# Performance work log

Hardware: AMD Instinct MI355X
Metric: run time of the kernel (lower is better)

## Reference

```python
import jax, jax.numpy as jnp
import numpy as np

S = 8          # num_slots
DSLOT = 128    # slot_dim
D_IN = 768     # input feature dim
ITERS = 3      # slot_att_iter
RES = 21       # 336 // 16
NGRID = RES * RES   # 441 grid positions
NTOK = 441          # tokens kept per frame (no drop here)
NFRAME = 2
F_ = 2 * NFRAME + 1  # 5 frames per clip
CLIPS = 8
B = CLIPS * F_       # 40
SIGMA = 5.0
SCALE = DSLOT ** -0.5
EPS = 1e-8


def layernorm(x, g, b):
    m = x.mean(-1, keepdims=True)
    v = ((x - m) ** 2).mean(-1, keepdims=True)
    return (x - m) * jax.lax.rsqrt(v + 1e-5) * g + b


def setup_inputs() -> dict:
    key = jax.random.key(0)
    ks = iter(jax.random.split(key, 64))
    def nrm(shape, s=0.02):
        return jax.random.normal(next(ks), shape, jnp.float32) * s
    xs = jnp.linspace(-1.0, 1.0, RES)
    ys = jnp.linspace(-1.0, 1.0, RES)
    gx, gy = jnp.meshgrid(xs, ys)  # indexing='xy' as in torch
    abs_grid = jnp.stack([gx.ravel(), gy.ravel()], axis=-1)  # [NGRID, 2]
    return {
        "inputs": jax.random.normal(next(ks), (B, NTOK, D_IN), jnp.float32),
        "token_indices": jnp.sort(jax.random.randint(next(ks), (B, NTOK), 0, NGRID), axis=-1),
        "abs_grid": abs_grid,
        "slots_init": nrm((1, S, DSLOT), 0.1),
        "S_p_init": nrm((1, S, 1, 2), 0.02),
        "S_s_init": jax.random.uniform(next(ks), (1, S, 1, 2), jnp.float32, 0.3, 0.7),
        "WQ": nrm((DSLOT, DSLOT)), "ln_g": jnp.ones((DSLOT,)), "ln_b": jnp.zeros((DSLOT,)),
        "gru_w_ih": nrm((DSLOT, 3 * DSLOT)), "gru_w_hh": nrm((DSLOT, 3 * DSLOT)),
        "gru_b_ih": jnp.zeros((3 * DSLOT,)), "gru_b_hh": jnp.zeros((3 * DSLOT,)),
        "mlp_ln_g": jnp.ones((DSLOT,)), "mlp_ln_b": jnp.zeros((DSLOT,)),
        "mlp_w1": nrm((DSLOT, 4 * DSLOT)), "mlp_b1": jnp.zeros((4 * DSLOT,)),
        "mlp_w2": nrm((4 * DSLOT, DSLOT)), "mlp_b2": jnp.zeros((DSLOT,)),
        "WK": nrm((DSLOT, DSLOT)), "WV": nrm((DSLOT, DSLOT)),
        "Wg": nrm((2, DSLOT)), "bg": jnp.zeros((DSLOT,)),
        "Wf1": nrm((DSLOT, DSLOT)), "bf1": jnp.zeros((DSLOT,)),
        "Wf2": nrm((DSLOT, DSLOT)), "bf2": jnp.zeros((DSLOT,)),
        "im_ln1_g": jnp.ones((D_IN,)), "im_ln1_b": jnp.zeros((D_IN,)),
        "im_w1": nrm((D_IN, D_IN)), "im_b1": jnp.zeros((D_IN,)),
        "im_w2": nrm((D_IN, DSLOT)), "im_b2": jnp.zeros((DSLOT,)),
        "im_ln2_g": jnp.ones((DSLOT,)), "im_ln2_b": jnp.zeros((DSLOT,)),
        "fin_w": nrm((DSLOT, DSLOT)), "fin_b": jnp.zeros((DSLOT,)),
    }


def _forward(inputs, token_indices, abs_grid, slots_init, S_p_init, S_s_init,
             WQ, ln_g, ln_b, gru_w_ih, gru_w_hh, gru_b_ih, gru_b_hh,
             mlp_ln_g, mlp_ln_b, mlp_w1, mlp_b1, mlp_w2, mlp_b2,
             WK, WV, Wg, bg, Wf1, bf1, Wf2, bf2,
             im_ln1_g, im_ln1_b, im_w1, im_b1, im_w2, im_b2, im_ln2_g, im_ln2_b,
             fin_w, fin_b):
    Bb = inputs.shape[0]
    # initial_mlp: LN -> Linear -> ReLU -> Linear -> LN
    x = layernorm(inputs, im_ln1_g, im_ln1_b)
    x = jax.nn.relu(x @ im_w1 + im_b1)
    x = x @ im_w2 + im_b2
    x = layernorm(x, im_ln2_g, im_ln2_b)          # [B, N, Dslot]
    # K/V projections of inputs are slot-independent; compute once.
    Kx = x @ WK                                    # [B, N, Dslot]
    Vx = x @ WV
    ag = abs_grid[token_indices]                   # [B, N, 2] per-batch gather
    slots = jnp.broadcast_to(slots_init, (Bb, S, DSLOT))
    S_p = jnp.broadcast_to(S_p_init, (Bb, S, 1, 2))
    S_s = jnp.broadcast_to(S_s_init, (Bb, S, 1, 2))

    def f_net(z):  # f = Linear -> ReLU -> Linear
        return jax.nn.relu(z @ Wf1 + bf1) @ Wf2 + bf2

    attn = None
    for t in range(ITERS + 1):
        slots_prev = slots
        sn = layernorm(slots, ln_g, ln_b)
        rel = (ag[:, None] - S_p) / (S_s * SIGMA)  # [B, S, N, 2]
        gr = rel @ Wg + bg                          # [B, S, N, Dslot]
        k = f_net(Kx[:, None] + gr)
        v = f_net(Vx[:, None] + gr)
        q = sn @ WQ                                 # [B, S, Dslot]
        dots = jnp.einsum('bsd,bsjd->bsj', q, k) * SCALE
        attn = jax.nn.softmax(dots, axis=1) + EPS   # softmax over slots
        attn = attn / attn.sum(-1, keepdims=True)   # renormalize over tokens
        updates = jnp.einsum('bsjd,bsj->bsd', v, attn)
        S_p = jnp.einsum('bjd,bsj->bsd', ag, attn)[:, :, None, :]
        S_s = jnp.sqrt(jnp.einsum('bsjd,bsj->bsd', (ag[:, None] - S_p) ** 2, attn))[:, :, None, :]
        if t != ITERS:
            # torch GRUCell
            xg = updates.reshape(-1, DSLOT)
            hg = slots_prev.reshape(-1, DSLOT)
            gi = xg @ gru_w_ih + gru_b_ih
            gh = hg @ gru_w_hh + gru_b_hh
            i_r, i_z, i_n = jnp.split(gi, 3, axis=-1)
            h_r, h_z, h_n = jnp.split(gh, 3, axis=-1)
            r = jax.nn.sigmoid(i_r + h_r)
            z = jax.nn.sigmoid(i_z + h_z)
            n = jnp.tanh(i_n + r * h_n)
            slots = ((1.0 - z) * n + z * hg).reshape(Bb, S, DSLOT)
            # residual pre-LN MLP (dropout is identity in eval)
            y = layernorm(slots, mlp_ln_g, mlp_ln_b)
            y = jax.nn.relu(y @ mlp_w1 + mlp_b1) @ mlp_w2 + mlp_b2
            slots = slots + y
    slots = slots @ fin_w + fin_b
    attn_out = attn.reshape(-1, F_, S, NTOK)[:, NFRAME]  # center frame
    return slots, attn_out


def reference(inputs, token_indices, abs_grid, slots_init, S_p_init, S_s_init,
              WQ, ln_g, ln_b, gru_w_ih, gru_w_hh, gru_b_ih, gru_b_hh,
              mlp_ln_g, mlp_ln_b, mlp_w1, mlp_b1, mlp_w2, mlp_b2,
              WK, WV, Wg, bg, Wf1, bf1, Wf2, bf2,
              im_ln1_g, im_ln1_b, im_w1, im_b1, im_w2, im_b2, im_ln2_g, im_ln2_b,
              fin_w, fin_b):
    return _forward(inputs, token_indices, abs_grid, slots_init, S_p_init, S_s_init,
                    WQ, ln_g, ln_b, gru_w_ih, gru_w_hh, gru_b_ih, gru_b_hh,
                    mlp_ln_g, mlp_ln_b, mlp_w1, mlp_b1, mlp_w2, mlp_b2,
                    WK, WV, Wg, bg, Wf1, bf1, Wf2, bf2,
                    im_ln1_g, im_ln1_b, im_w1, im_b1, im_w2, im_b2, im_ln2_g, im_ln2_b,
                    fin_w, fin_b)
```

## Files before the change

kernel.cpp:

```cpp
#include <hip/hip_runtime.h>
#include <cstdio>

#define NB 40
#define NS 8
#define NT 441
#define DIN 768
#define DD 128
#define NTOT (NB*NT)
#define FSCALE 0.08838834764831843f

typedef short s8v __attribute__((ext_vector_type(8)));
typedef float f4v __attribute__((ext_vector_type(4)));

__device__ inline ushort f2bf(float f){
  unsigned u = __float_as_uint(f);
  unsigned r = (u + 0x7fffu + ((u >> 16) & 1u)) >> 16;
  return (ushort)r;
}
__device__ inline float bf2f(ushort h){ return __uint_as_float(((unsigned)h) << 16); }
__device__ inline float dot4a(float4 a, float4 b, float acc){
  return fmaf(a.w, b.w, fmaf(a.z, b.z, fmaf(a.y, b.y, fmaf(a.x, b.x, acc))));
}

struct PP {
  const float *inputs; const int *tok_idx; const float *abs_grid;
  const float *slots_init, *Sp_init, *Ss_init;
  const float *WQ, *ln_g, *ln_b;
  const float *gru_w_ih, *gru_w_hh, *gru_b_ih, *gru_b_hh;
  const float *mlp_ln_g, *mlp_ln_b, *mlp_w1, *mlp_b1, *mlp_w2, *mlp_b2;
  const float *WK, *WV, *Wg, *bg, *Wf1, *bf1, *Wf2, *bf2;
  const float *im_ln1_g, *im_ln1_b, *im_w1, *im_b1, *im_w2, *im_b2, *im_ln2_g, *im_ln2_b;
  const float *fin_w, *fin_b;
  float *A_K, *A_V, *Wg1, *c1, *Wf2T;
  float *slots_g, *qw_g, *qb_g, *spss_g, *hpart_g, *a_g;
  float4 *WQp, *f2P, *f2TP, *finP, *gihP, *ghhP, *w1P, *w2P;
  ushort *xnh, *xnl, *hh, *hl, *W1Th, *W1Tl, *W2Th, *W2Tl;
  ushort *WKfTh, *WKfTl, *WVfTh, *WVfTl;
  float *out;
};

__global__ __launch_bounds__(128) void prep_weights(PP p){
  int r = blockIdx.x, d = threadIdx.x;
  float accK = 0.f, accV = 0.f;
  for (int kk = 0; kk < DD; kk++){
    float w = p.Wf1[kk*DD + d];
    accK = fmaf(p.WK[r*DD+kk], w, accK);
    accV = fmaf(p.WV[r*DD+kk], w, accV);
  }
  ushort hk = f2bf(accK), hv = f2bf(accV);
  p.WKfTh[d*DD + r] = hk; p.WKfTl[d*DD + r] = f2bf(accK - bf2f(hk));
  p.WVfTh[d*DD + r] = hv; p.WVfTl[d*DD + r] = f2bf(accV - bf2f(hv));
  if (r < 2){
    float a = 0.f;
    for (int kk = 0; kk < DD; kk++) a = fmaf(p.Wg[r*DD+kk], p.Wf1[kk*DD+d], a);
    p.Wg1[r*DD+d] = a;
  }
  if (r == 2){
    float a = 0.f;
    for (int kk = 0; kk < DD; kk++) a = fmaf(p.bg[kk], p.Wf1[kk*DD+d], a);
    p.c1[d] = a + p.bf1[d];
  }
  p.Wf2T[d*DD + r] = p.Wf2[r*DD + d];
}

__global__ __launch_bounds__(256) void prep_pack(PP p){
  long i = (long)blockIdx.x*256 + threadIdx.x;
  const float* src; float4* dst; int N; long base;
  if      (i < 4096) { src = p.WQ;        dst = p.WQp;  N = 128; base = 0; }
  else if (i < 8192) { src = p.Wf2;       dst = p.f2P;  N = 128; base = 4096; }
  else if (i < 12288){ src = p.Wf2T;      dst = p.f2TP; N = 128; base = 8192; }
  else if (i < 16384){ src = p.fin_w;     dst = p.finP; N = 128; base = 12288; }
  else if (i < 28672){ src = p.gru_w_ih;  dst = p.gihP; N = 384; base = 16384; }
  else if (i < 40960){ src = p.gru_w_hh;  dst = p.ghhP; N = 384; base = 28672; }
  else if (i < 57344){ src = p.mlp_w1;    dst = p.w1P;  N = 512; base = 40960; }
  else               { src = p.mlp_w2;    dst = p.w2P;  N = 128; base = 57344; }
  long j = i - base;
  long k4 = j / N, o = j % N;
  float4 v;
  v.x = src[(k4*4+0)*N+o]; v.y = src[(k4*4+1)*N+o];
  v.z = src[(k4*4+2)*N+o]; v.w = src[(k4*4+3)*N+o];
  dst[j] = v;
}

__global__ __launch_bounds__(256) void transpose_both(PP p){
  __shared__ float tile[64][65];
  int t = blockIdx.x;
  const float* W; ushort *WTh, *WTl; int N, k0, n0;
  if (t < 144){ W = p.im_w1; WTh = p.W1Th; WTl = p.W1Tl; N = 768; k0 = (t/12)*64; n0 = (t%12)*64; }
  else { t -= 144; W = p.im_w2; WTh = p.W2Th; WTl = p.W2Tl; N = 128; k0 = (t/2)*64; n0 = (t&1)*64; }
  int tid = threadIdx.x;
  #pragma unroll
  for (int i = 0; i < 4; i++){
    int k = i*16 + (tid >> 4);
    int n4 = (tid & 15) * 4;
    float4 v = *(const float4*)(W + (long)(k0+k)*N + n0 + n4);
    tile[k][n4+0] = v.x; tile[k][n4+1] = v.y; tile[k][n4+2] = v.z; tile[k][n4+3] = v.w;
  }
  __syncthreads();
  #pragma unroll
  for (int i = 0; i < 4; i++){
    int n = i*16 + (tid >> 4);
    int k4 = (tid & 15) * 4;
    ushort4 h4, l4;
    float v0 = tile[k4+0][n], v1 = tile[k4+1][n], v2 = tile[k4+2][n], v3 = tile[k4+3][n];
    h4.x = f2bf(v0); l4.x = f2bf(v0 - bf2f(h4.x));
    h4.y = f2bf(v1); l4.y = f2bf(v1 - bf2f(h4.y));
    h4.z = f2bf(v2); l4.z = f2bf(v2 - bf2f(h4.z));
    h4.w = f2bf(v3); l4.w = f2bf(v3 - bf2f(h4.w));
    *(ushort4*)(WTh + (long)(n0+n)*DIN + k0 + k4) = h4;
    *(ushort4*)(WTl + (long)(n0+n)*DIN + k0 + k4) = l4;
  }
}

__device__ void phase0g(const PP& p, int bs, int tid, float* scr, const float* sl,
                        float Sp0, float Sp1, float Ss0, float Ss1){
  float* sn   = scr;
  float* qv   = scr + 128;
  float* part = scr + 256;
  float* red  = scr + 512;
  int o = tid & 127, h = tid >> 7;
  float v = (tid < 128) ? sl[tid] : 0.f;
  float s1 = v, s2 = v*v;
  #pragma unroll
  for (int m = 1; m < 64; m <<= 1){ s1 += __shfl_xor(s1,m); s2 += __shfl_xor(s2,m); }
  if (tid < 128 && (tid & 63) == 0){ red[(tid>>6)*2] = s1; red[(tid>>6)*2+1] = s2; }
  __syncthreads();
  float mean = (red[0]+red[2])*(1.f/128.f);
  float var  = (red[1]+red[3])*(1.f/128.f) - mean*mean;
  float rstd = rsqrtf(var + 1e-5f);
  if (tid < 128) sn[tid] = (v-mean)*rstd*p.ln_g[tid] + p.ln_b[tid];
  __syncthreads();
  float acc = 0.f;
  for (int k4 = 0; k4 < 16; k4++){
    float4 sv = *(const float4*)&sn[h*64 + k4*4];
    float4 wv = p.WQp[(h*16 + k4)*128 + o];
    acc = dot4a(sv, wv, acc);
  }
  part[h*128+o] = acc;
  __syncthreads();
  if (tid < 128) qv[tid] = part[tid] + part[128+tid];
  __syncthreads();
  float acc2 = 0.f;
  for (int k4 = 0; k4 < 16; k4++){
    float4 qv4 = *(const float4*)&qv[h*64 + k4*4];
    float4 wv  = p.f2TP[(h*16 + k4)*128 + o];
    acc2 = dot4a(qv4, wv, acc2);
  }
  part[h*128+o] = acc2;
  __syncthreads();
  if (tid < 128) p.qw_g[(long)bs*128+tid] = part[tid] + part[128+tid];
  float pb = (tid < 128) ? qv[tid]*p.bf2[tid] : 0.f;
  #pragma unroll
  for (int m = 1; m < 64; m <<= 1) pb += __shfl_xor(pb,m);
  if ((tid & 63) == 0) red[4 + (tid>>6)] = pb;
  __syncthreads();
  if (tid == 0){
    p.qb_g[bs] = FSCALE*(red[4]+red[5]+red[6]+red[7]);
    p.spss_g[bs*4+0] = Sp0; p.spss_g[bs*4+1] = Sp1;
    p.spss_g[bs*4+2] = 1.f/(Ss0*5.0f); p.spss_g[bs*4+3] = 1.f/(Ss1*5.0f);
  }
}

__global__ __launch_bounds__(256) void ln1_init(PP p){
  __shared__ __align__(16) float sl[128];
  __shared__ __align__(16) float scr[520];
  if (blockIdx.x < 4410){
    int tok = blockIdx.x*4 + (threadIdx.x >> 6);
    int l = threadIdx.x & 63;
    const float* src = p.inputs + (long)tok*DIN;
    float4 v[3];
    float s = 0.f, s2 = 0.f;
    #pragma unroll
    for (int pp = 0; pp < 3; pp++){
      v[pp] = *(const float4*)(src + pp*256 + l*4);
      s  += v[pp].x + v[pp].y + v[pp].z + v[pp].w;
      s2 += v[pp].x*v[pp].x + v[pp].y*v[pp].y + v[pp].z*v[pp].z + v[pp].w*v[pp].w;
    }
    #pragma unroll
    for (int m = 1; m < 64; m <<= 1){ s += __shfl_xor(s, m); s2 += __shfl_xor(s2, m); }
    float mean = s*(1.f/DIN), var = s2*(1.f/DIN) - mean*mean;
    float rstd = rsqrtf(var + 1e-5f);
    #pragma unroll
    for (int pp = 0; pp < 3; pp++){
      int idx = pp*256 + l*4;
      float4 g = *(const float4*)(p.im_ln1_g + idx);
      float4 b = *(const float4*)(p.im_ln1_b + idx);
      float y0 = (v[pp].x-mean)*rstd*g.x + b.x;
      float y1 = (v[pp].y-mean)*rstd*g.y + b.y;
      float y2 = (v[pp].z-mean)*rstd*g.z + b.z;
      float y3 = (v[pp].w-mean)*rstd*g.w + b.w;
      ushort4 h4, l4;
      h4.x = f2bf(y0); l4.x = f2bf(y0 - bf2f(h4.x));
      h4.y = f2bf(y1); l4.y = f2bf(y1 - bf2f(h4.y));
      h4.z = f2bf(y2); l4.z = f2bf(y2 - bf2f(h4.z));
      h4.w = f2bf(y3); l4.w = f2bf(y3 - bf2f(h4.w));
      *(ushort4*)(p.xnh + (long)tok*DIN + idx) = h4;
      *(ushort4*)(p.xnl + (long)tok*DIN + idx) = l4;
    }
  } else {
    int bs = blockIdx.x - 4410, ss = bs & 7, tid = threadIdx.x;
    if (tid < 128){
      float v = p.slots_init[ss*128+tid];
      sl[tid] = v;
      p.slots_g[(long)bs*128+tid] = v;
    }
    __syncthreads();
    phase0g(p, bs, tid, scr, sl,
            p.Sp_init[ss*2], p.Sp_init[ss*2+1], p.Ss_init[ss*2], p.Ss_init[ss*2+1]);
  }
}

__global__ __launch_bounds__(256, 2) void gemm1_128(PP p){
  __shared__ __align__(16) ushort LDSm[32768];
  int id = blockIdx.x;
  int xcd = id & 7, idx = id >> 3;
  int m_t = xcd + 8*(idx/6), n_t = idx % 6;
  if (m_t >= 138) return;
  int m0 = m_t*128, n0 = n_t*128;
  int tid = threadIdx.x;
  int w = tid >> 6, lane = tid & 63;
  int wm = w >> 1, wn = w & 1;
  int lch = lane ^ ((lane >> 3) & 7);
  int r_in = lch >> 2, kgs = lch & 3;
  const ushort* S = (w == 0) ? p.xnh : (w == 1) ? p.xnl : (w == 2) ? p.W1Th : p.W1Tl;
  int base0 = (w < 2) ? m0 : n0;
  bool isA = (w < 2);
  int kg = lane >> 4, rA = lane & 15;
  int cc = rA*4 + kg;
  int cs = cc ^ ((cc >> 3) & 7);
  const char* LB = (const char*)LDSm;

  f4v acc[4][4];
  #pragma unroll
  for (int mf = 0; mf < 4; mf++)
    #pragma unroll
    for (int nf = 0; nf < 4; nf++) acc[mf][nf] = (f4v)(0.f);

  #pragma unroll
  for (int t = 0; t < 8; t++){
    int grow = base0 + t*16 + r_in;
    if (isA) grow = min(grow, NTOT-1);
    const ushort* gptr = S + (long)grow*DIN + 0 + kgs*8;
    ushort* lptr = &LDSm[w*4096 + t*512];
    __builtin_amdgcn_global_load_lds(
        (const __attribute__((address_space(1))) void*)gptr,
        (__attribute__((address_space(3))) void*)lptr, 16, 0, 0);
  }
  __syncthreads();

  int cur = 0;
  for (int kb = 0; kb < DIN; kb += 32){
    if (kb + 32 < DIN){
      int nb = cur ^ 1;
      #pragma unroll
      for (int t = 0; t < 8; t++){
        int grow = base0 + t*16 + r_in;
        if (isA) grow = min(grow, NTOT-1);
        const ushort* gptr = S + (long)grow*DIN + (kb + 32) + kgs*8;
        ushort* lptr = &LDSm[nb*16384 + w*4096 + t*512];
        __builtin_amdgcn_global_load_lds(
            (const __attribute__((address_space(1))) void*)gptr,
            (__attribute__((address_space(3))) void*)lptr, 16, 0, 0);
      }
    }
    const char* B = LB + cur*32768;
    s8v a0[4], a1[4], b0[4], b1[4];
    #pragma unroll
    for (int mf = 0; mf < 4; mf++){
      int win = wm*4 + mf;
      a0[mf] = *(const s8v*)(B +         win*1024 + cs*16);
      a1[mf] = *(const s8v*)(B +  8192 + win*1024 + cs*16);
    }
    #pragma unroll
    for (int nf = 0; nf < 4; nf++){
      int win = wn*4 + nf;
      b0[nf] = *(const s8v*)(B + 16384 + win*1024 + cs*16);
      b1[nf] = *(const s8v*)(B + 24576 + win*1024 + cs*16);
    }
    #pragma unroll
    for (int mf = 0; mf < 4; mf++)
      #pragma unroll
      for (int nf = 0; nf < 4; nf++){
        acc[mf][nf] = __builtin_amdgcn_mfma_f32_16x16x32_bf16(a0[mf], b0[nf], acc[mf][nf], 0, 0, 0);
        acc[mf][nf] = __builtin_amdgcn_mfma_f32_16x16x32_bf16(a0[mf], b1[nf], acc[mf][nf], 0, 0, 0);
        acc[mf][nf] = __builtin_amdgcn_mfma_f32_16x16x32_bf16(a1[mf], b0[nf], acc[mf][nf], 0, 0, 0);
      }
    __syncthreads();
    cur ^= 1;
  }

  int rbase = (lane >> 4) * 4, cn = lane & 15;
  #pragma unroll
  for (int mf = 0; mf < 4; mf++)
    #pragma unroll
    for (int nf = 0; nf < 4; nf++){
      int n = n0 + wn*64 + nf*16 + cn;
      float bs = p.im_b1[n];
      #pragma unroll
      for (int r = 0; r < 4; r++){
        int m = m0 + wm*64 + mf*16 + rbase + r;
        if (m < NTOT){
          float v = fmaxf(acc[mf][nf][r] + bs, 0.f);
          ushort h = f2bf(v);
          p.hh[(long)m*DIN + n] = h;
          p.hl[(long)m*DIN + n] = f2bf(v - bf2f(h));
        }
      }
    }
}

__global__ __launch_bounds__(256) void gemm2_fused(PP p){
  __shared__ __align__(16) char smem[43008];
  ushort* As = (ushort*)smem;
  ushort* Bs = (ushort*)(smem + 5120);
  float*  Dl = (float*)smem;
  ushort* xsh = (ushort*)(smem + 25600);
  ushort* xsl = (ushort*)(smem + 25600 + 8704);
  int m0 = blockIdx.x * 32;
  int tid = threadIdx.x, w = tid >> 6, lane = tid & 63;
  f4v acc[2][2];
  #pragma unroll
  for (int mf = 0; mf < 2; mf++)
    #pragma unroll
    for (int nf = 0; nf < 2; nf++) acc[mf][nf] = (f4v)(0.f);

  for (int kb = 0; kb < DIN; kb += 32){
    __syncthreads();
    {
      int c = tid;
      int s = c >> 7, rem = c & 127, r = rem >> 2, kg = rem & 3;
      int gr = min(m0 + r, NTOT-1);
      const float4 va = *(const float4*)((s ? p.hl : p.hh) + (long)gr*DIN + kb + kg*8);
      *(float4*)(As + s*1280 + r*40 + kg*8) = va;
    }
    #pragma unroll
    for (int i = 0; i < 4; i++){
      int c = tid + i*256;
      int s = c >> 9, r = (c >> 2) & 127, kg = c & 3;
      const float4 vb = *(const float4*)((s ? p.W2Tl : p.W2Th) + (long)r*DIN + kb + kg*8);
      *(float4*)(Bs + s*5120 + r*40 + kg*8) = vb;
    }
    __syncthreads();
    int kg = lane >> 4, rA = lane & 15;
    s8v a0[2], a1[2], b0[2], b1[2];
    #pragma unroll
    for (int mf = 0; mf < 2; mf++){
      a0[mf] = *(const s8v*)(As +        (mf*16 + rA)*40 + kg*8);
      a1[mf] = *(const s8v*)(As + 1280 + (mf*16 + rA)*40 + kg*8);
    }
    #pragma unroll
    for (int nf = 0; nf < 2; nf++){
      int rb = w*32 + nf*16 + rA;
      b0[nf] = *(const s8v*)(Bs +        rb*40 + kg*8);
      b1[nf] = *(const s8v*)(Bs + 5120 + rb*40 + kg*8);
    }
    #pragma unroll
    for (int mf = 0; mf < 2; mf++)
      #pragma unroll
      for (int nf = 0; nf < 2; nf++){
        acc[mf][nf] = __builtin_amdgcn_mfma_f32_16x16x32_bf16(a0[mf], b0[nf], acc[mf][nf], 0, 0, 0);
        acc[mf][nf] = __builtin_amdgcn_mfma_f32_16x16x32_bf16(a0[mf], b1[nf], acc[mf][nf], 0, 0, 0);
        acc[mf][nf] = __builtin_amdgcn_mfma_f32_16x16x32_bf16(a1[mf], b0[nf], acc[mf][nf], 0, 0, 0);
      }
  }

  int rbase = (lane >> 4) * 4, cn = lane & 15;
  __syncthreads();
  #pragma unroll
  for (int mf = 0; mf < 2; mf++)
    #pragma unroll
    for (int nf = 0; nf < 2; nf++){
      int n = w*32 + nf*16 + cn;
      float bs = p.im_b2[n];
      #pragma unroll
      for (int r = 0; r < 4; r++)
        Dl[(mf*16 + rbase + r)*132 + n] = acc[mf][nf][r] + bs;
    }
  __syncthreads();
  for (int rr = 0; rr < 8; rr++){
    int row = w*8 + rr;
    float e0 = Dl[row*132 + lane], e1 = Dl[row*132 + 64 + lane];
    float s = e0 + e1, s2 = e0*e0 + e1*e1;
    #pragma unroll
    for (int m2 = 1; m2 < 64; m2 <<= 1){ s += __shfl_xor(s, m2); s2 += __shfl_xor(s2, m2); }
    float mean = s*(1.f/DD), var = s2*(1.f/DD) - mean*mean;
    float rstd = rsqrtf(var + 1e-5f);
    float x0 = (e0-mean)*rstd*p.im_ln2_g[lane]    + p.im_ln2_b[lane];
    float x1 = (e1-mean)*rstd*p.im_ln2_g[64+lane] + p.im_ln2_b[64+lane];
    ushort h0 = f2bf(x0), h1 = f2bf(x1);
    xsh[row*136 + lane]      = h0;  xsl[row*136 + lane]      = f2bf(x0 - bf2f(h0));
    xsh[row*136 + 64 + lane] = h1;  xsl[row*136 + 64 + lane] = f2bf(x1 - bf2f(h1));
  }
  __syncthreads();
  int kg = lane >> 4, rA = lane & 15;
  int kv = w >> 1, rowblk = w & 1;
  const ushort* WTh = kv ? p.WVfTh : p.WKfTh;
  const ushort* WTl = kv ? p.WVfTl : p.WKfTl;
  float* OUT = kv ? p.A_V : p.A_K;
  f4v aO[8];
  #pragma unroll
  for (int nf = 0; nf < 8; nf++) aO[nf] = (f4v)(0.f);
  #pragma unroll
  for (int kb2 = 0; kb2 < 4; kb2++){
    s8v ah = *(const s8v*)&xsh[(rowblk*16+rA)*136 + kb2*32 + kg*8];
    s8v al = *(const s8v*)&xsl[(rowblk*16+rA)*136 + kb2*32 + kg*8];
    #pragma unroll
    for (int nf = 0; nf < 8; nf++){
      int n = nf*16 + rA;
      s8v bh = *(const s8v*)(WTh + n*DD + kb2*32 + kg*8);
      s8v bl = *(const s8v*)(WTl + n*DD + kb2*32 + kg*8);
      aO[nf] = __builtin_amdgcn_mfma_f32_16x16x32_bf16(ah, bh, aO[nf], 0, 0, 0);
      aO[nf] = __builtin_amdgcn_mfma_f32_16x16x32_bf16(ah, bl, aO[nf], 0, 0, 0);
      aO[nf] = __builtin_amdgcn_mfma_f32_16x16x32_bf16(al, bh, aO[nf], 0, 0, 0);
    }
  }
  #pragma unroll
  for (int nf = 0; nf < 8; nf++){
    int n = nf*16 + cn;
    float c = p.c1[n];
    #pragma unroll
    for (int r = 0; r < 4; r++){
      int m = m0 + rowblk*16 + rbase + r;
      if (m < NTOT) OUT[(long)m*DD + n] = aO[nf][r] + c;
    }
  }
}

template<int LAST>
__global__ __launch_bounds__(256) void kA(PP p){
  int b = blockIdx.x / 7, tile = blockIdx.x % 7;
  int tid = threadIdx.x, wid = tid >> 6, lane = tid & 63;
  __shared__ float qws[8][132];
  __shared__ float qbs[8];
  __shared__ float spssL[32];
  __shared__ float agt[64][2];
  __shared__ float a_tile[8][64];
  __shared__ float hpartL[4][8][128];
  for (int f = tid; f < 8*128; f += 256){
    int s = f >> 7, d = f & 127;
    qws[s][(d&31)*4 + (d>>5)] = p.qw_g[((long)b*8+s)*128 + d];
  }
  if (tid < 8)  qbs[tid] = p.qb_g[b*8+tid];
  if (tid < 32) spssL[tid] = p.spss_g[b*32+tid];
  if (tid < 64){
    int j = tile*64 + tid;
    float g0 = 0.f, g1 = 0.f;
    if (j < NT){ int idx = p.tok_idx[b*NT+j]; g0 = p.abs_grid[idx*2]; g1 = p.abs_grid[idx*2+1]; }
    agt[tid][0] = g0; agt[tid][1] = g1;
  }
  __syncthreads();

  {
    int tl = lane >> 2, dg = lane & 3;
    int jtok = wid*16 + tl, j = tile*64 + jtok;
    bool valid = j < NT;
    int jc = valid ? j : 0;
    float aa[32], w0[32], w1[32];
    const float* src = p.A_K + ((long)(b*NT+jc))*DD + dg*32;
    #pragma unroll
    for (int i4 = 0; i4 < 8; i4++){
      float4 t = *(const float4*)(src + i4*4);
      aa[i4*4+0]=t.x; aa[i4*4+1]=t.y; aa[i4*4+2]=t.z; aa[i4*4+3]=t.w;
    }
    #pragma unroll
    for (int i4 = 0; i4 < 8; i4++){
      float4 t0 = *(const float4*)(p.Wg1 + dg*32 + i4*4);
      float4 t1 = *(const float4*)(p.Wg1 + DD + dg*32 + i4*4);
      w0[i4*4+0]=t0.x; w0[i4*4+1]=t0.y; w0[i4*4+2]=t0.z; w0[i4*4+3]=t0.w;
      w1[i4*4+0]=t1.x; w1[i4*4+1]=t1.y; w1[i4*4+2]=t1.z; w1[i4*4+3]=t1.w;
    }
    float ag0 = agt[jtok][0], ag1 = agt[jtok][1];
    float dv[8];
    #pragma unroll
    for (int s = 0; s < 8; s++){
      float rel0 = (ag0 - spssL[s*4+0])*spssL[s*4+2];
      float rel1 = (ag1 - spssL[s*4+1])*spssL[s*4+3];
      float acc = 0.f;
      #pragma unroll
      for (int i = 0; i < 32; i++){
        float hk = fmaxf(fmaf(rel0, w0[i], fmaf(rel1, w1[i], aa[i])), 0.f);
        acc = fmaf(hk, qws[s][i*4+dg], acc);
      }
      acc += __shfl_xor(acc, 1); acc += __shfl_xor(acc, 2);
      dv[s] = acc*FSCALE + qbs[s];
    }
    if (dg == 0){
      float m = -1e30f;
      #pragma unroll
      for (int s = 0; s < 8; s++) m = fmaxf(m, dv[s]);
      float tot = 0.f;
      #pragma unroll
      for (int s = 0; s < 8; s++){ dv[s] = expf(dv[s]-m); tot += dv[s]; }
      float inv = 1.f/tot;
      #pragma unroll
      for (int s = 0; s < 8; s++)
        a_tile[s][jtok] = valid ? (dv[s]*inv + 1e-8f) : 0.f;
    }
  }
  __syncthreads();

  #pragma unroll
  for (int si = 0; si < 2; si++){
    int s = wid*2 + si;
    float a = a_tile[s][lane];
    float g0 = agt[lane][0], g1 = agt[lane][1];
    float v0 = a, v1 = a*g0, v2 = a*g1, v3 = a*g0*g0, v4 = a*g1*g1;
    #pragma unroll
    for (int m = 1; m < 64; m <<= 1){
      v0 += __shfl_xor(v0,m); v1 += __shfl_xor(v1,m); v2 += __shfl_xor(v2,m);
      v3 += __shfl_xor(v3,m); v4 += __shfl_xor(v4,m);
    }
    if (lane == 0){
      float* st = p.hpart_g + ((long)(b*7+tile)*8 + s)*136 + 128;
      st[0]=v0; st[1]=v1; st[2]=v2; st[3]=v3; st[4]=v4;
    }
  }

  if (LAST){
    if ((b % 5) == 2){
      int clip = b/5;
      for (int f = tid; f < 8*64; f += 256){
        int s = f >> 6, jt = f & 63;
        int j = tile*64 + jt;
        if (j < NT) p.a_g[((long)clip*8 + s)*NT + j] = a_tile[s][jt];
      }
    }
    return;
  }

  {
    float sp0[8], sp1[8], si0[8], si1[8];
    #pragma unroll
    for (int s = 0; s < 8; s++){
      sp0[s]=spssL[s*4+0]; sp1[s]=spssL[s*4+1]; si0[s]=spssL[s*4+2]; si1[s]=spssL[s*4+3];
    }
    int d0 = lane, d1 = lane + 64;
    float wg0a = p.Wg1[d0], wg1a = p.Wg1[DD+d0];
    float wg0b = p.Wg1[d1], wg1b = p.Wg1[DD+d1];
    float acc0[8], acc1[8];
    #pragma unroll
    for (int s = 0; s < 8; s++){ acc0[s]=0.f; acc1[s]=0.f; }
    for (int jj = wid; jj < 64; jj += 4){
      int j = tile*64 + jj;
      if (j >= NT) continue;
      float av0 = p.A_V[((long)(b*NT+j))*DD + d0];
      float av1 = p.A_V[((long)(b*NT+j))*DD + d1];
      float g0 = agt[jj][0], g1 = agt[jj][1];
      #pragma unroll
      for (int s = 0; s < 8; s++){
        float rel0 = (g0 - sp0[s])*si0[s];
        float rel1 = (g1 - sp1[s])*si1[s];
        float a = a_tile[s][jj];
        float hv0 = fmaxf(fmaf(rel0, wg0a, fmaf(rel1, wg1a, av0)), 0.f);
        float hv1 = fmaxf(fmaf(rel0, wg0b, fmaf(rel1, wg1b, av1)), 0.f);
        acc0[s] = fmaf(a, hv0, acc0[s]);
        acc1[s] = fmaf(a, hv1, acc1[s]);
      }
    }
    #pragma unroll
    for (int s = 0; s < 8; s++){ hpartL[wid][s][d0] = acc0[s]; hpartL[wid][s][d1] = acc1[s]; }
    __syncthreads();
    for (int f = tid; f < 1024; f += 256){
      int s = f >> 7, d = f & 127;
      p.hpart_g[((long)(b*7+tile)*8 + s)*136 + d] =
        hpartL[0][s][d] + hpartL[1][s][d] + hpartL[2][s][d] + hpartL[3][s][d];
    }
  }
}

template<int LAST>
__global__ __launch_bounds__(256) void kB(PP p){
  __shared__ __align__(16) float red[8];
  __shared__ __align__(16) float sl[128];
  __shared__ __align__(16) float hb[128];
  __shared__ __align__(16) float scr[2304];
  int bs = blockIdx.x, b = bs >> 3, ss = bs & 7, tid = threadIdx.x;
  if (tid < 5){
    float v = 0.f;
    #pragma unroll
    for (int t7 = 0; t7 < 7; t7++) v += p.hpart_g[((long)(b*7+t7)*8 + ss)*136 + 128 + tid];
    red[tid] = v;
  }
  __syncthreads();
  float SA = red[0], inv = 1.f/SA;
  float Sp0 = red[1]*inv, Sp1 = red[2]*inv;
  float Ss0 = sqrtf(fmaxf(red[3]*inv - Sp0*Sp0, 0.f));
  float Ss1 = sqrtf(fmaxf(red[4]*inv - Sp1*Sp1, 0.f));

  if (LAST){
    if ((b % 5) == 2){
      int clip = b/5;
      long base = (long)NB*NS*DD + ((long)clip*8 + ss)*NT;
      const float* arow = p.a_g + ((long)clip*8 + ss)*NT;
      for (int j = tid; j < NT; j += 256) p.out[base+j] = arow[j]*inv;
    }
    if (tid < 128) sl[tid] = p.slots_g[(long)bs*128+tid];
    __syncthreads();
    int o = tid & 127, h = tid >> 7;
    float acc = 0.f;
    for (int k4 = 0; k4 < 16; k4++){
      float4 sv = *(const float4*)&sl[h*64 + k4*4];
      float4 wv = p.finP[(h*16 + k4)*128 + o];
      acc = dot4a(sv, wv, acc);
    }
    scr[h*128+o] = acc;
    __syncthreads();
    if (tid < 128) p.out[(long)bs*128+tid] = p.fin_b[tid] + scr[tid] + scr[128+tid];
    return;
  }

  if (tid < 128){
    float v = 0.f;
    #pragma unroll
    for (int t7 = 0; t7 < 7; t7++) v += p.hpart_g[((long)(b*7+t7)*8 + ss)*136 + tid];
    hb[tid] = v * inv;
    sl[tid] = p.slots_g[(long)bs*128+tid];
  }
  __syncthreads();
  float* part = scr;
  float* upd  = scr + 256;
  float* gil  = scr + 384;
  float* ghl  = scr + 768;
  float* hnl  = scr + 1152;
  float* yv   = scr + 1280;
  float* h1   = scr + 1408;
  int o = tid & 127, h = tid >> 7;
  float acc2 = 0.f;
  for (int k4 = 0; k4 < 16; k4++){
    float4 hv = *(const float4*)&hb[h*64 + k4*4];
    float4 wv = p.f2P[(h*16 + k4)*128 + o];
    acc2 = dot4a(hv, wv, acc2);
  }
  part[h*128+o] = acc2;
  __syncthreads();
  if (tid < 128) upd[tid] = part[tid] + part[128+tid] + p.bf2[tid];
  __syncthreads();
  int oA = tid, oB = tid + 256;
  float giA = p.gru_b_ih[oA], ghA = p.gru_b_hh[oA];
  float giB = 0.f, ghB = 0.f;
  if (tid < 128){ giB = p.gru_b_ih[oB]; ghB = p.gru_b_hh[oB]; }
  for (int k4 = 0; k4 < 32; k4++){
    float4 u4 = *(const float4*)&upd[k4*4];
    float4 s4 = *(const float4*)&sl[k4*4];
    float4 wiA = p.gihP[k4*384 + oA];
    float4 whA = p.ghhP[k4*384 + oA];
    giA = dot4a(u4, wiA, giA);
    ghA = dot4a(s4, whA, ghA);
    if (tid < 128){
      float4 wiB = p.gihP[k4*384 + oB];
      float4 whB = p.ghhP[k4*384 + oB];
      giB = dot4a(u4, wiB, giB);
      ghB = dot4a(s4, whB, ghB);
    }
  }
  gil[oA] = giA; ghl[oA] = ghA;
  if (tid < 128){ gil[oB] = giB; ghl[oB] = ghB; }
  __syncthreads();
  float hnv = 0.f;
  if (tid < 128){
    float r = 1.f/(1.f+expf(-(gil[tid]+ghl[tid])));
    float z = 1.f/(1.f+expf(-(gil[128+tid]+ghl[128+tid])));
    float n = tanhf(gil[256+tid] + r*ghl[256+tid]);
    hnv = (1.f-z)*n + z*sl[tid];
  }
  float t1 = hnv, t2 = hnv*hnv;
  #pragma unroll
  for (int m = 1; m < 64; m <<= 1){ t1 += __shfl_xor(t1,m); t2 += __shfl_xor(t2,m); }
  if (tid < 128 && (tid & 63) == 0){ red[(tid>>6)*2] = t1; red[(tid>>6)*2+1] = t2; }
  __syncthreads();
  float mean = (red[0]+red[2])*(1.f/128.f);
  float var  = (red[1]+red[3])*(1.f/128.f) - mean*mean;
  float rstd = rsqrtf(var + 1e-5f);
  if (tid < 128){
    hnl[tid] = hnv;
    yv[tid] = (hnv-mean)*rstd*p.mlp_ln_g[tid] + p.mlp_ln_b[tid];
  }
  __syncthreads();
  float m1A = p.mlp_b1[tid], m1B = p.mlp_b1[tid+256];
  for (int k4 = 0; k4 < 32; k4++){
    float4 y4 = *(const float4*)&yv[k4*4];
    float4 wA = p.w1P[k4*512 + tid];
    float4 wB = p.w1P[k4*512 + tid + 256];
    m1A = dot4a(y4, wA, m1A);
    m1B = dot4a(y4, wB, m1B);
  }
  h1[tid] = fmaxf(m1A, 0.f); h1[tid+256] = fmaxf(m1B, 0.f);
  __syncthreads();
  float a2 = 0.f;
  for (int k4 = 0; k4 < 64; k4++){
    float4 h4 = *(const float4*)&h1[h*256 + k4*4];
    float4 wv = p.w2P[(h*64 + k4)*128 + o];
    a2 = dot4a(h4, wv, a2);
  }
  part[h*128+o] = a2;
  __syncthreads();
  if (tid < 128){
    float sln = hnl[tid] + p.mlp_b2[tid] + part[tid] + part[128+tid];
    sl[tid] = sln;
    p.slots_g[(long)bs*128+tid] = sln;
  }
  __syncthreads();
  phase0g(p, bs, tid, scr, sl, Sp0, Sp1, Ss0, Ss1);
}

extern "C" void kernel_launch(void* const* d_in, const int* in_sizes, int n_in,
                              void* d_out, int out_size, void* d_ws, size_t ws_size,
                              hipStream_t stream){
  PP p;
  p.inputs=(const float*)d_in[0]; p.tok_idx=(const int*)d_in[1]; p.abs_grid=(const float*)d_in[2];
  p.slots_init=(const float*)d_in[3]; p.Sp_init=(const float*)d_in[4]; p.Ss_init=(const float*)d_in[5];
  p.WQ=(const float*)d_in[6]; p.ln_g=(const float*)d_in[7]; p.ln_b=(const float*)d_in[8];
  p.gru_w_ih=(const float*)d_in[9]; p.gru_w_hh=(const float*)d_in[10];
  p.gru_b_ih=(const float*)d_in[11]; p.gru_b_hh=(const float*)d_in[12];
  p.mlp_ln_g=(const float*)d_in[13]; p.mlp_ln_b=(const float*)d_in[14];
  p.mlp_w1=(const float*)d_in[15]; p.mlp_b1=(const float*)d_in[16];
  p.mlp_w2=(const float*)d_in[17]; p.mlp_b2=(const float*)d_in[18];
  p.WK=(const float*)d_in[19]; p.WV=(const float*)d_in[20]; p.Wg=(const float*)d_in[21]; p.bg=(const float*)d_in[22];
  p.Wf1=(const float*)d_in[23]; p.bf1=(const float*)d_in[24]; p.Wf2=(const float*)d_in[25]; p.bf2=(const float*)d_in[26];
  p.im_ln1_g=(const float*)d_in[27]; p.im_ln1_b=(const float*)d_in[28];
  p.im_w1=(const float*)d_in[29]; p.im_b1=(const float*)d_in[30];
  p.im_w2=(const float*)d_in[31]; p.im_b2=(const float*)d_in[32];
  p.im_ln2_g=(const float*)d_in[33]; p.im_ln2_b=(const float*)d_in[34];
  p.fin_w=(const float*)d_in[35]; p.fin_b=(const float*)d_in[36];

  float* w = (float*)d_ws;
  size_t need = 0;
  auto alloc = [&](size_t nfl){ nfl = (nfl + 3) & ~(size_t)3; float* r = w + need; need += nfl; return r; };
  p.A_K  = alloc((size_t)NTOT*DD);
  p.A_V  = alloc((size_t)NTOT*DD);
  p.Wg1  = alloc(2*DD);
  p.c1   = alloc(DD);
  p.Wf2T = alloc(DD*DD);
  p.slots_g = alloc(320*128);
  p.qw_g    = alloc(320*128);
  p.qb_g    = alloc(320);
  p.spss_g  = alloc(320*4);
  p.hpart_g = alloc((size_t)NB*7*8*136);
  p.a_g     = alloc((size_t)8*8*NT);
  p.WQp  = (float4*)alloc(4096*4);
  p.f2P  = (float4*)alloc(4096*4);
  p.f2TP = (float4*)alloc(4096*4);
  p.finP = (float4*)alloc(4096*4);
  p.gihP = (float4*)alloc(12288*4);
  p.ghhP = (float4*)alloc(12288*4);
  p.w1P  = (float4*)alloc(16384*4);
  p.w2P  = (float4*)alloc(16384*4);
  p.xnh  = (ushort*)alloc((size_t)NTOT*DIN/2);
  p.xnl  = (ushort*)alloc((size_t)NTOT*DIN/2);
  p.hh   = (ushort*)alloc((size_t)NTOT*DIN/2);
  p.hl   = (ushort*)alloc((size_t)NTOT*DIN/2);
  p.W1Th = (ushort*)alloc((size_t)DIN*DIN/2);
  p.W1Tl = (ushort*)alloc((size_t)DIN*DIN/2);
  p.W2Th = (ushort*)alloc((size_t)DD*DIN/2);
  p.W2Tl = (ushort*)alloc((size_t)DD*DIN/2);
  p.WKfTh = (ushort*)alloc(DD*DD/2);
  p.WKfTl = (ushort*)alloc(DD*DD/2);
  p.WVfTh = (ushort*)alloc(DD*DD/2);
  p.WVfTl = (ushort*)alloc(DD*DD/2);
  p.out = (float*)d_out;
  if (ws_size < need*sizeof(float)){
    fprintf(stderr, "kernel_launch: ws too small (%zu < %zu)\n", ws_size, need*sizeof(float));
    return;
  }

  prep_weights<<<dim3(DD), dim3(128), 0, stream>>>(p);
  prep_pack<<<dim3(288), dim3(256), 0, stream>>>(p);
  transpose_both<<<dim3(168), dim3(256), 0, stream>>>(p);
  ln1_init<<<dim3(4730), dim3(256), 0, stream>>>(p);
  gemm1_128<<<dim3(832), dim3(256), 0, stream>>>(p);
  gemm2_fused<<<dim3((NTOT+31)/32), dim3(256), 0, stream>>>(p);

  for (int t = 0; t < 3; t++){
    kA<0><<<dim3(NB*7), dim3(256), 0, stream>>>(p);
    kB<0><<<dim3(320), dim3(256), 0, stream>>>(p);
  }
  kA<1><<<dim3(NB*7), dim3(256), 0, stream>>>(p);
  kB<1><<<dim3(320), dim3(256), 0, stream>>>(p);
}
```

Measured before the change: 411.9 us.

## Fuse attention and slot-update kernels with per-batch atomic counters

```diff
diff --git a/kernel.cpp b/kernel.cpp
--- a/kernel.cpp
+++ b/kernel.cpp
@@ -34,6 +34,7 @@
   float *A_K, *A_V, *Wg1, *c1, *Wf2T;
   float *slots_g, *qw_g, *qb_g, *spss_g, *hpart_g, *a_g;
   float4 *WQp, *f2P, *f2TP, *finP, *gihP, *ghhP, *w1P, *w2P;
+  int *bar;
   ushort *xnh, *xnl, *hh, *hl, *W1Th, *W1Tl, *W2Th, *W2Tl;
   ushort *WKfTh, *WKfTl, *WVfTh, *WVfTl;
   float *out;
@@ -41,6 +42,7 @@
 
 __global__ __launch_bounds__(128) void prep_weights(PP p){
   int r = blockIdx.x, d = threadIdx.x;
+  if (r < 2 && d < 80) p.bar[r*80 + d] = 0;
   float accK = 0.f, accV = 0.f;
   for (int kk = 0; kk < DD; kk++){
     float w = p.Wf1[kk*DD + d];
@@ -427,154 +429,167 @@
 }
 
 template<int LAST>
-__global__ __launch_bounds__(256) void kA(PP p){
-  int b = blockIdx.x / 7, tile = blockIdx.x % 7;
+__global__ __launch_bounds__(256) void kAB(PP p, int tno){
+  __shared__ __align__(16) float smem[5832];
   int tid = threadIdx.x, wid = tid >> 6, lane = tid & 63;
-  __shared__ float qws[8][132];
-  __shared__ float qbs[8];
-  __shared__ float spssL[32];
-  __shared__ float agt[64][2];
-  __shared__ float a_tile[8][64];
-  __shared__ float hpartL[4][8][128];
-  for (int f = tid; f < 8*128; f += 256){
-    int s = f >> 7, d = f & 127;
-    qws[s][(d&31)*4 + (d>>5)] = p.qw_g[((long)b*8+s)*128 + d];
-  }
-  if (tid < 8)  qbs[tid] = p.qb_g[b*8+tid];
-  if (tid < 32) spssL[tid] = p.spss_g[b*32+tid];
-  if (tid < 64){
-    int j = tile*64 + tid;
-    float g0 = 0.f, g1 = 0.f;
-    if (j < NT){ int idx = p.tok_idx[b*NT+j]; g0 = p.abs_grid[idx*2]; g1 = p.abs_grid[idx*2+1]; }
-    agt[tid][0] = g0; agt[tid][1] = g1;
-  }
-  __syncthreads();
-
-  {
-    int tl = lane >> 2, dg = lane & 3;
-    int jtok = wid*16 + tl, j = tile*64 + jtok;
-    bool valid = j < NT;
-    int jc = valid ? j : 0;
-    float aa[32], w0[32], w1[32];
-    const float* src = p.A_K + ((long)(b*NT+jc))*DD + dg*32;
-    #pragma unroll
-    for (int i4 = 0; i4 < 8; i4++){
-      float4 t = *(const float4*)(src + i4*4);
-      aa[i4*4+0]=t.x; aa[i4*4+1]=t.y; aa[i4*4+2]=t.z; aa[i4*4+3]=t.w;
-    }
-    #pragma unroll
-    for (int i4 = 0; i4 < 8; i4++){
-      float4 t0 = *(const float4*)(p.Wg1 + dg*32 + i4*4);
-      float4 t1 = *(const float4*)(p.Wg1 + DD + dg*32 + i4*4);
-      w0[i4*4+0]=t0.x; w0[i4*4+1]=t0.y; w0[i4*4+2]=t0.z; w0[i4*4+3]=t0.w;
-      w1[i4*4+0]=t1.x; w1[i4*4+1]=t1.y; w1[i4*4+2]=t1.z; w1[i4*4+3]=t1.w;
-    }
-    float ag0 = agt[jtok][0], ag1 = agt[jtok][1];
-    float dv[8];
-    #pragma unroll
-    for (int s = 0; s < 8; s++){
-      float rel0 = (ag0 - spssL[s*4+0])*spssL[s*4+2];
-      float rel1 = (ag1 - spssL[s*4+1])*spssL[s*4+3];
-      float acc = 0.f;
-      #pragma unroll
-      for (int i = 0; i < 32; i++){
-        float hk = fmaxf(fmaf(rel0, w0[i], fmaf(rel1, w1[i], aa[i])), 0.f);
-        acc = fmaf(hk, qws[s][i*4+dg], acc);
-      }
-      acc += __shfl_xor(acc, 1); acc += __shfl_xor(acc, 2);
-      dv[s] = acc*FSCALE + qbs[s];
-    }
-    if (dg == 0){
-      float m = -1e30f;
-      #pragma unroll
-      for (int s = 0; s < 8; s++) m = fmaxf(m, dv[s]);
-      float tot = 0.f;
-      #pragma unroll
-      for (int s = 0; s < 8; s++){ dv[s] = expf(dv[s]-m); tot += dv[s]; }
-      float inv = 1.f/tot;
-      #pragma unroll
-      for (int s = 0; s < 8; s++)
-        a_tile[s][jtok] = valid ? (dv[s]*inv + 1e-8f) : 0.f;
-    }
-  }
-  __syncthreads();
-
-  #pragma unroll
-  for (int si = 0; si < 2; si++){
-    int s = wid*2 + si;
-    float a = a_tile[s][lane];
-    float g0 = agt[lane][0], g1 = agt[lane][1];
-    float v0 = a, v1 = a*g0, v2 = a*g1, v3 = a*g0*g0, v4 = a*g1*g1;
-    #pragma unroll
-    for (int m = 1; m < 64; m <<= 1){
-      v0 += __shfl_xor(v0,m); v1 += __shfl_xor(v1,m); v2 += __shfl_xor(v2,m);
-      v3 += __shfl_xor(v3,m); v4 += __shfl_xor(v4,m);
-    }
-    if (lane == 0){
-      float* st = p.hpart_g + ((long)(b*7+tile)*8 + s)*136 + 128;
-      st[0]=v0; st[1]=v1; st[2]=v2; st[3]=v3; st[4]=v4;
-    }
-  }
-
-  if (LAST){
-    if ((b % 5) == 2){
-      int clip = b/5;
-      for (int f = tid; f < 8*64; f += 256){
-        int s = f >> 6, jt = f & 63;
-        int j = tile*64 + jt;
-        if (j < NT) p.a_g[((long)clip*8 + s)*NT + j] = a_tile[s][jt];
-      }
+  int* bar = p.bar + tno*40;
+
+  if (blockIdx.x < 280){
+    int b = blockIdx.x / 7, tile = blockIdx.x % 7;
+    float* qws   = smem;
+    float* qbs   = smem + 1056;
+    float* spssL = smem + 1064;
+    float* agt   = smem + 1096;
+    float* a_tile= smem + 1224;
+    float* hpartL= smem + 1736;
+    for (int f = tid; f < 8*128; f += 256){
+      int s = f >> 7, d = f & 127;
+      qws[s*132 + (d&31)*4 + (d>>5)] = p.qw_g[((long)b*8+s)*128 + d];
+    }
+    if (tid < 8)  qbs[tid] = p.qb_g[b*8+tid];
+    if (tid < 32) spssL[tid] = p.spss_g[b*32+tid];
+    if (tid < 64){
+      int j = tile*64 + tid;
+      float g0 = 0.f, g1 = 0.f;
+      if (j < NT){ int idx = p.tok_idx[b*NT+j]; g0 = p.abs_grid[idx*2]; g1 = p.abs_grid[idx*2+1]; }
+      agt[tid*2+0] = g0; agt[tid*2+1] = g1;
+    }
+    __syncthreads();
+
+    {
+      int tl = lane >> 2, dg = lane & 3;
+      int jtok = wid*16 + tl, j = tile*64 + jtok;
+      bool valid = j < NT;
+      int jc = valid ? j : 0;
+      float aa[32], w0[32], w1[32];
+      const float* src = p.A_K + ((long)(b*NT+jc))*DD + dg*32;
+      #pragma unroll
+      for (int i4 = 0; i4 < 8; i4++){
+        float4 t = *(const float4*)(src + i4*4);
+        aa[i4*4+0]=t.x; aa[i4*4+1]=t.y; aa[i4*4+2]=t.z; aa[i4*4+3]=t.w;
+      }
+      #pragma unroll
+      for (int i4 = 0; i4 < 8; i4++){
+        float4 t0 = *(const float4*)(p.Wg1 + dg*32 + i4*4);
+        float4 t1 = *(const float4*)(p.Wg1 + DD + dg*32 + i4*4);
+        w0[i4*4+0]=t0.x; w0[i4*4+1]=t0.y; w0[i4*4+2]=t0.z; w0[i4*4+3]=t0.w;
+        w1[i4*4+0]=t1.x; w1[i4*4+1]=t1.y; w1[i4*4+2]=t1.z; w1[i4*4+3]=t1.w;
+      }
+      float ag0 = agt[jtok*2+0], ag1 = agt[jtok*2+1];
+      float dv[8];
+      #pragma unroll
+      for (int s = 0; s < 8; s++){
+        float rel0 = (ag0 - spssL[s*4+0])*spssL[s*4+2];
+        float rel1 = (ag1 - spssL[s*4+1])*spssL[s*4+3];
+        float acc = 0.f;
+        #pragma unroll
+        for (int i = 0; i < 32; i++){
+          float hk = fmaxf(fmaf(rel0, w0[i], fmaf(rel1, w1[i], aa[i])), 0.f);
+          acc = fmaf(hk, qws[s*132 + i*4+dg], acc);
+        }
+        acc += __shfl_xor(acc, 1); acc += __shfl_xor(acc, 2);
+        dv[s] = acc*FSCALE + qbs[s];
+      }
+      if (dg == 0){
+        float m = -1e30f;
+        #pragma unroll
+        for (int s = 0; s < 8; s++) m = fmaxf(m, dv[s]);
+        float tot = 0.f;
+        #pragma unroll
+        for (int s = 0; s < 8; s++){ dv[s] = expf(dv[s]-m); tot += dv[s]; }
+        float inv = 1.f/tot;
+        #pragma unroll
+        for (int s = 0; s < 8; s++)
+          a_tile[s*64 + jtok] = valid ? (dv[s]*inv + 1e-8f) : 0.f;
+      }
+    }
+    __syncthreads();
+
+    #pragma unroll
+    for (int si = 0; si < 2; si++){
+      int s = wid*2 + si;
+      float a = a_tile[s*64 + lane];
+      float g0 = agt[lane*2+0], g1 = agt[lane*2+1];
+      float v0 = a, v1 = a*g0, v2 = a*g1, v3 = a*g0*g0, v4 = a*g1*g1;
+      #pragma unroll
+      for (int m = 1; m < 64; m <<= 1){
+        v0 += __shfl_xor(v0,m); v1 += __shfl_xor(v1,m); v2 += __shfl_xor(v2,m);
+        v3 += __shfl_xor(v3,m); v4 += __shfl_xor(v4,m);
+      }
+      if (lane == 0){
+        float* st = p.hpart_g + ((long)(b*7+tile)*8 + s)*136 + 128;
+        st[0]=v0; st[1]=v1; st[2]=v2; st[3]=v3; st[4]=v4;
+      }
+    }
+
+    if (!LAST){
+      float sp0[8], sp1[8], si0[8], si1[8];
+      #pragma unroll
+      for (int s = 0; s < 8; s++){
+        sp0[s]=spssL[s*4+0]; sp1[s]=spssL[s*4+1]; si0[s]=spssL[s*4+2]; si1[s]=spssL[s*4+3];
+      }
+      int d0 = lane, d1 = lane + 64;
+      float wg0a = p.Wg1[d0], wg1a = p.Wg1[DD+d0];
+      float wg0b = p.Wg1[d1], wg1b = p.Wg1[DD+d1];
+      float acc0[8], acc1[8];
+      #pragma unroll
+      for (int s = 0; s < 8; s++){ acc0[s]=0.f; acc1[s]=0.f; }
+      for (int jj = wid; jj < 64; jj += 4){
+        int j = tile*64 + jj;
+        if (j >= NT) continue;
+        float av0 = p.A_V[((long)(b*NT+j))*DD + d0];
+        float av1 = p.A_V[((long)(b*NT+j))*DD + d1];
+        float g0 = agt[jj*2+0], g1 = agt[jj*2+1];
+        #pragma unroll
+        for (int s = 0; s < 8; s++){
+          float rel0 = (g0 - sp0[s])*si0[s];
+          float rel1 = (g1 - sp1[s])*si1[s];
+          float a = a_tile[s*64 + jj];
+          float hv0 = fmaxf(fmaf(rel0, wg0a, fmaf(rel1, wg1a, av0)), 0.f);
+          float hv1 = fmaxf(fmaf(rel0, wg0b, fmaf(rel1, wg1b, av1)), 0.f);
+          acc0[s] = fmaf(a, hv0, acc0[s]);
+          acc1[s] = fmaf(a, hv1, acc1[s]);
+        }
+      }
+      #pragma unroll
+      for (int s = 0; s < 8; s++){ hpartL[(wid*8+s)*128 + d0] = acc0[s]; hpartL[(wid*8+s)*128 + d1] = acc1[s]; }
+      __syncthreads();
+      for (int f = tid; f < 1024; f += 256){
+        int s = f >> 7, d = f & 127;
+        p.hpart_g[((long)(b*7+tile)*8 + s)*136 + d] =
+          hpartL[s*128+d] + hpartL[1024 + s*128+d] + hpartL[2048 + s*128+d] + hpartL[3072 + s*128+d];
+      }
+    } else {
+      if ((b % 5) == 2){
+        int clip = b/5;
+        for (int f = tid; f < 8*64; f += 256){
+          int s = f >> 6, jt = f & 63;
+          int j = tile*64 + jt;
+          if (j < NT) p.a_g[((long)clip*8 + s)*NT + j] = a_tile[s*64 + jt];
+        }
+      }
+    }
+    __syncthreads();
+    if (tid == 0){
+      __threadfence();
+      atomicAdd(&bar[b], 1);
     }
     return;
   }
 
-  {
-    float sp0[8], sp1[8], si0[8], si1[8];
-    #pragma unroll
-    for (int s = 0; s < 8; s++){
-      sp0[s]=spssL[s*4+0]; sp1[s]=spssL[s*4+1]; si0[s]=spssL[s*4+2]; si1[s]=spssL[s*4+3];
-    }
-    int d0 = lane, d1 = lane + 64;
-    float wg0a = p.Wg1[d0], wg1a = p.Wg1[DD+d0];
-    float wg0b = p.Wg1[d1], wg1b = p.Wg1[DD+d1];
-    float acc0[8], acc1[8];
-    #pragma unroll
-    for (int s = 0; s < 8; s++){ acc0[s]=0.f; acc1[s]=0.f; }
-    for (int jj = wid; jj < 64; jj += 4){
-      int j = tile*64 + jj;
-      if (j >= NT) continue;
-      float av0 = p.A_V[((long)(b*NT+j))*DD + d0];
-      float av1 = p.A_V[((long)(b*NT+j))*DD + d1];
-      float g0 = agt[jj][0], g1 = agt[jj][1];
-      #pragma unroll
-      for (int s = 0; s < 8; s++){
-        float rel0 = (g0 - sp0[s])*si0[s];
-        float rel1 = (g1 - sp1[s])*si1[s];
-        float a = a_tile[s][jj];
-        float hv0 = fmaxf(fmaf(rel0, wg0a, fmaf(rel1, wg1a, av0)), 0.f);
-        float hv1 = fmaxf(fmaf(rel0, wg0b, fmaf(rel1, wg1b, av1)), 0.f);
-        acc0[s] = fmaf(a, hv0, acc0[s]);
-        acc1[s] = fmaf(a, hv1, acc1[s]);
-      }
-    }
-    #pragma unroll
-    for (int s = 0; s < 8; s++){ hpartL[wid][s][d0] = acc0[s]; hpartL[wid][s][d1] = acc1[s]; }
-    __syncthreads();
-    for (int f = tid; f < 1024; f += 256){
-      int s = f >> 7, d = f & 127;
-      p.hpart_g[((long)(b*7+tile)*8 + s)*136 + d] =
-        hpartL[0][s][d] + hpartL[1][s][d] + hpartL[2][s][d] + hpartL[3][s][d];
-    }
-  }
-}
-
-template<int LAST>
-__global__ __launch_bounds__(256) void kB(PP p){
-  __shared__ __align__(16) float red[8];
-  __shared__ __align__(16) float sl[128];
-  __shared__ __align__(16) float hb[128];
-  __shared__ __align__(16) float scr[2304];
-  int bs = blockIdx.x, b = bs >> 3, ss = bs & 7, tid = threadIdx.x;
+  int bs = blockIdx.x - 280, b = bs >> 3, ss = bs & 7;
+  float* red = smem;
+  float* sl  = smem + 8;
+  float* hb  = smem + 136;
+  float* scr = smem + 264;
+
+  if (tid == 0){
+    while (__hip_atomic_load(&bar[b], __ATOMIC_RELAXED, __HIP_MEMORY_SCOPE_AGENT) < 7)
+      __builtin_amdgcn_s_sleep(2);
+    (void)__hip_atomic_load(&bar[b], __ATOMIC_ACQUIRE, __HIP_MEMORY_SCOPE_AGENT);
+  }
+  __syncthreads();
+
   if (tid < 5){
     float v = 0.f;
     #pragma unroll
@@ -745,6 +760,7 @@
   p.ghhP = (float4*)alloc(12288*4);
   p.w1P  = (float4*)alloc(16384*4);
   p.w2P  = (float4*)alloc(16384*4);
+  p.bar  = (int*)alloc(160);
   p.xnh  = (ushort*)alloc((size_t)NTOT*DIN/2);
   p.xnl  = (ushort*)alloc((size_t)NTOT*DIN/2);
   p.hh   = (ushort*)alloc((size_t)NTOT*DIN/2);
@@ -770,10 +786,7 @@
   gemm1_128<<<dim3(832), dim3(256), 0, stream>>>(p);
   gemm2_fused<<<dim3((NTOT+31)/32), dim3(256), 0, stream>>>(p);
 
-  for (int t = 0; t < 3; t++){
-    kA<0><<<dim3(NB*7), dim3(256), 0, stream>>>(p);
-    kB<0><<<dim3(320), dim3(256), 0, stream>>>(p);
-  }
-  kA<1><<<dim3(NB*7), dim3(256), 0, stream>>>(p);
-  kB<1><<<dim3(320), dim3(256), 0, stream>>>(p);
-}
+  for (int t = 0; t < 3; t++)
+    kAB<0><<<dim3(600), dim3(256), 0, stream>>>(p, t);
+  kAB<1><<<dim3(600), dim3(256), 0, stream>>>(p, 3);
+}
```

Result: slower. 443.9 us (+7.8%).
